# Performance work log

Hardware: AMD Instinct MI355X
Metric: run time of the kernel (lower is better)

## Reference

```python
import jax, jax.numpy as jnp
import numpy as np

B, C_IN, C_OUT, N, K = 4, 128, 128, 4096, 32
BN_EPS = 1e-5


def setup_inputs() -> dict:
    key = jax.random.key(0)
    ks = jax.random.split(key, 12)
    x = jax.random.normal(ks[0], (B, C_IN, N), jnp.float32)
    feature = jax.random.normal(ks[1], (B, C_OUT, N, K), jnp.float32)
    graph_index = jax.random.randint(ks[2], (B, N, K), 0, N)
    s_in = 1.0 / np.sqrt(C_IN)
    s_out = 1.0 / np.sqrt(C_OUT)
    # theta_x: Conv2d(C_IN -> C_IN, 1x1), shared for theta and phi branches
    Wt = jax.random.uniform(ks[3], (C_IN, C_IN), jnp.float32, -s_in, s_in)
    bt = jax.random.uniform(ks[4], (C_IN,), jnp.float32, -s_in, s_in)
    # g: Conv2d(C_OUT -> C_OUT, 1x1)
    Wg = jax.random.uniform(ks[5], (C_OUT, C_OUT), jnp.float32, -s_out, s_out)
    bg = jax.random.uniform(ks[6], (C_OUT,), jnp.float32, -s_out, s_out)
    # W: Conv1d(C_OUT -> C_OUT, 1) followed by BatchNorm1d(C_OUT)
    Ww = jax.random.uniform(ks[7], (C_OUT, C_OUT), jnp.float32, -s_out, s_out)
    bw = jax.random.uniform(ks[8], (C_OUT,), jnp.float32, -s_out, s_out)
    gamma = jnp.ones((C_OUT,), jnp.float32)
    beta = jnp.zeros((C_OUT,), jnp.float32)
    return {"graph_index": graph_index, "x": x, "feature": feature,
            "Wt": Wt, "bt": bt, "Wg": Wg, "bg": bg,
            "Ww": Ww, "bw": bw, "gamma": gamma, "beta": beta}


def reference(graph_index, x, feature, Wt, bt, Wg, bg, Ww, bw, gamma, beta):
    b, c, n = x.shape
    # torch does x.contiguous().view(B, N, C) -> a reshape, not a transpose
    xr = x.reshape(b, n, c)                                   # [B,N,C]
    # index_points: per-batch gather of k neighbors
    batch_idx = jnp.arange(b)[:, None, None]
    nb = xr[batch_idx, graph_index]                           # [B,N,K,C]
    # theta_x 1x1 conv applied to centre and to neighbors (shared weights)
    theta = jnp.einsum('bnc,dc->bnd', xr, Wt) + bt            # [B,N,C]
    phi = jnp.einsum('bnkc,dc->bnkd', nb, Wt) + bt            # [B,N,K,C]
    # local attention logits over k neighbors, softmax over k
    logits = jnp.einsum('bnd,bnkd->bnk', theta, phi)          # [B,N,K]
    coef = jax.nn.softmax(logits, axis=-1)                    # [B,N,K]
    # g 1x1 conv on neighbor value features
    gx = jnp.einsum('bcnk,dc->bnkd', feature, Wg) + bg        # [B,N,K,Cout]
    # weighted aggregation over neighbors
    out = jnp.einsum('bnk,bnkd->bnd', coef, gx)               # [B,N,Cout]
    # W: 1x1 Conv1d then BatchNorm1d (training-mode batch stats)
    y = jnp.einsum('bnd,ed->ben', out, Ww) + bw[None, :, None]  # [B,Cout,N]
    mean = jnp.mean(y, axis=(0, 2), keepdims=True)
    var = jnp.var(y, axis=(0, 2), keepdims=True)
    z = (y - mean) * jax.lax.rsqrt(var + BN_EPS)
    z = z * gamma[None, :, None] + beta[None, :, None]
    return z
```

## Files before the change

kernel.cpp:

```cpp
#include <hip/hip_runtime.h>
#include <hip/hip_bf16.h>

#define BB 4
#define CC 128
#define NN 4096
#define KK 32
#define THETA_OFF 0
#define THETA_SZ  (BB*NN*CC)
#define AGG_OFF   (THETA_OFF + THETA_SZ)
#define AGG_SZ    (BB*NN*CC)
#define M_OFF     (AGG_OFF + AGG_SZ)
#define M_SZ      (CC*CC)
#define B2_OFF    (M_OFF + M_SZ)
#define COEF_OFF  (B2_OFF + 128)
#define COEF_SZ   (BB*NN*KK)
#define PART_OFF  (COEF_OFF + COEF_SZ)
#define PART_SZ   (512*256)
#define PART2_OFF (PART_OFF + PART_SZ)
#define PART2_SZ  (64*256)
#define STAT_OFF  (PART2_OFF + PART2_SZ)

__device__ __forceinline__ float dot4(float4 a, float4 b) {
    return a.x*b.x + a.y*b.y + a.z*b.z + a.w*b.w;
}

__device__ __forceinline__ void async_copy16(const float* g, float* l) {
    __builtin_amdgcn_global_load_lds(
        (const __attribute__((address_space(1))) void*)g,
        (__attribute__((address_space(3))) void*)l, 16, 0, 0);
}

#define SYNCB() do { asm volatile("" ::: "memory"); \
                     __builtin_amdgcn_s_barrier(); \
                     asm volatile("" ::: "memory"); } while (0)

__global__ __launch_bounds__(256) void kWT(const float* __restrict__ x,
                                           const float* __restrict__ Wt,
                                           const float* __restrict__ bt,
                                           const float* __restrict__ Ww,
                                           const float* __restrict__ Wg,
                                           const float* __restrict__ bg,
                                           const float* __restrict__ bw,
                                           float* __restrict__ theta,
                                           float* __restrict__ M,
                                           float* __restrict__ b2) {
    __shared__ float xr[32][132];
    __shared__ float wt[128][36];
    int t = threadIdx.x;
    if (blockIdx.x >= 512) {
        int bid2 = blockIdx.x - 512;
        if (bid2 < 64) {
            int e = bid2 * 2 + (t >> 7);
            int c = t & 127;
            float acc = 0.f;
#pragma unroll 8
            for (int d = 0; d < 128; ++d)
                acc += Ww[e*128 + d] * Wg[d*128 + c];
            M[e*128 + c] = acc;
        } else if (t < 128) {
            float acc = bw[t];
            for (int d = 0; d < 128; ++d)
                acc += Ww[t*128 + d] * bg[d];
            b2[t] = acc;
        }
        return;
    }
    long base = (long)blockIdx.x * (32 * 128);
#pragma unroll
    for (int r = 0; r < 4; ++r) {
        int f = (t + 256*r) * 4;
        int dn = f >> 7, c = f & 127;
        *(float4*)&xr[dn][c] = *(const float4*)(x + base + f);
    }
    float acc[4][4] = {};
    int e0 = t & 31, dn0 = (t >> 5) * 4;
    for (int cb = 0; cb < 4; ++cb) {
        __syncthreads();
#pragma unroll
        for (int r = 0; r < 4; ++r) {
            int f = (t + 256*r) * 4;
            int d = f >> 5, cc = f & 31;
            *(float4*)&wt[d][cc] = *(const float4*)(Wt + d*128 + cb*32 + cc);
        }
        __syncthreads();
#pragma unroll
        for (int q = 0; q < 8; ++q) {
            float4 a4[4], m4[4];
#pragma unroll
            for (int j = 0; j < 4; ++j) a4[j] = *(const float4*)&xr[dn0+j][cb*32 + q*4];
#pragma unroll
            for (int i = 0; i < 4; ++i) m4[i] = *(const float4*)&wt[e0 + 32*i][q*4];
#pragma unroll
            for (int i = 0; i < 4; ++i)
#pragma unroll
                for (int j = 0; j < 4; ++j)
                    acc[i][j] += dot4(a4[j], m4[i]);
        }
    }
    __syncthreads();
#pragma unroll
    for (int i = 0; i < 4; ++i) {
        float b = bt[e0 + 32*i];
#pragma unroll
        for (int j = 0; j < 4; ++j)
            xr[dn0 + j][e0 + 32*i] = acc[i][j] + b;
    }
    __syncthreads();
#pragma unroll
    for (int r = 0; r < 4; ++r) {
        int f = (t + 256*r) * 4;
        int dn = f >> 7, c = f & 127;
        *(float4*)(theta + base + f) = *(const float4*)&xr[dn][c];
    }
}

__global__ __launch_bounds__(256) void kA(const int* __restrict__ gi,
                                          const float* __restrict__ theta,
                                          float* __restrict__ coefG) {
    __shared__ float tc[16][132];
    __shared__ float logits[16][33];
    int t = threadIdx.x;
    int bid = (blockIdx.x & 7) * 128 + (blockIdx.x >> 3);
    long trow0 = (long)bid * 16;
    int b = bid >> 8;
    int k = t >> 3, l8 = t & 7;
#pragma unroll
    for (int r = 0; r < 2; ++r) {
        int f = (t + 256*r) * 4;
        int dn = f >> 7, c = f & 127;
        *(float4*)&tc[dn][c] = *(const float4*)(theta + trow0*128 + f);
    }
    int idxs[16];
#pragma unroll
    for (int dn = 0; dn < 16; ++dn)
        idxs[dn] = gi[(trow0 + dn) * KK + k];
    __syncthreads();
    const float* tbat = theta + (long)b * NN * CC;
#pragma unroll 2
    for (int dn = 0; dn < 16; ++dn) {
        const float* row = tbat + (long)idxs[dn] * CC;
        float p = 0.f;
#pragma unroll
        for (int j = 0; j < 4; ++j) {
            int c = j*32 + l8*4;
            float4 g = *(const float4*)(row + c);
            float4 tcv = *(const float4*)&tc[dn][c];
            p += dot4(g, tcv);
        }
        p += __shfl_xor(p, 1);
        p += __shfl_xor(p, 2);
        p += __shfl_xor(p, 4);
        if (l8 == 0) logits[dn][k] = p;
    }
    __syncthreads();
    if (t < 128) {
        int row = t >> 3;
        float l[4];
#pragma unroll
        for (int j = 0; j < 4; ++j) l[j] = logits[row][l8 + 8*j];
        float m = fmaxf(fmaxf(l[0], l[1]), fmaxf(l[2], l[3]));
        m = fmaxf(m, __shfl_xor(m, 1));
        m = fmaxf(m, __shfl_xor(m, 2));
        m = fmaxf(m, __shfl_xor(m, 4));
        float e[4]; float s = 0.f;
#pragma unroll
        for (int j = 0; j < 4; ++j) { e[j] = __expf(l[j] - m); s += e[j]; }
        s += __shfl_xor(s, 1);
        s += __shfl_xor(s, 2);
        s += __shfl_xor(s, 4);
        float inv = 1.0f / s;
#pragma unroll
        for (int j = 0; j < 4; ++j)
            coefG[(trow0 + row) * KK + l8 + 8*j] = e[j] * inv;
    }
}

__global__ __launch_bounds__(256) void kB(const float* __restrict__ coefG,
                                          const float* __restrict__ feat,
                                          float* __restrict__ aggG) {
    __shared__ float stage[3][4][32][32];
    __shared__ float aggL[32][36];
    int t = threadIdx.x;
    int cc4 = blockIdx.x & 3;
    int tile = blockIdx.x >> 2;
    int b = tile >> 7;
    int n0 = (tile & 127) * 32;
    int dn = t >> 3, l8 = t & 7;
    int w = t >> 6, lane = t & 63;

    float4 cf = *(const float4*)(coefG + ((size_t)tile * 32 + dn) * KK + l8 * 4);
    asm volatile("" :: "v"(cf.x), "v"(cf.y), "v"(cf.z), "v"(cf.w));

    const size_t S = (size_t)NN * KK;
    const float* fbase = feat + ((size_t)b * CC + cc4 * 32) * S + (size_t)n0 * KK + lane * 4;

#pragma unroll
    for (int ch = 0; ch < 3; ++ch) {
        const float* fc = fbase + (size_t)(ch * 4 + w) * S;
        float* ld = &stage[ch][w][0][0];
#pragma unroll
        for (int i = 0; i < 4; ++i)
            async_copy16(fc + i * 256, ld + i * 256);
    }

    int slot = 0;
#pragma unroll
    for (int ch = 0; ch < 8; ++ch) {
        int rem = 7 - ch;
        if (rem >= 2)      asm volatile("s_waitcnt vmcnt(8)" ::: "memory");
        else if (rem == 1) asm volatile("s_waitcnt vmcnt(4)" ::: "memory");
        else               asm volatile("s_waitcnt vmcnt(0)" ::: "memory");
        SYNCB();
#pragma unroll
        for (int cl = 0; cl < 4; ++cl) {
            float4 f = *(const float4*)&stage[slot][cl][dn][l8 * 4];
            float v = dot4(f, cf);
            v += __shfl_xor(v, 1);
            v += __shfl_xor(v, 2);
            v += __shfl_xor(v, 4);
            if (l8 == 0) aggL[dn][ch * 4 + cl] = v;
        }
        SYNCB();
        if (ch + 3 < 8) {
            const float* fc = fbase + (size_t)((ch + 3) * 4 + w) * S;
            float* ld = &stage[slot][w][0][0];
#pragma unroll
            for (int i = 0; i < 4; ++i)
                async_copy16(fc + i * 256, ld + i * 256);
        }
        slot = (slot == 2) ? 0 : slot + 1;
    }
    __syncthreads();
    int row = t >> 3, col4 = l8 * 4;
    *(float4*)(aggG + ((size_t)b * NN + n0 + row) * CC + cc4 * 32 + col4) =
        *(const float4*)&aggL[row][col4];
}

__global__ __launch_bounds__(256) void kC(const float* __restrict__ aggG,
                                          const float* __restrict__ Mmat,
                                          const float* __restrict__ b2v,
                                          float* __restrict__ y,
                                          float* __restrict__ partial) {
    __shared__ float agg[32][132];
    __shared__ float mc[128][36];
    __shared__ float pw[4][128];
    __shared__ float qw[4][128];
    int t = threadIdx.x;
    int b = blockIdx.x >> 7;
    int n0 = (blockIdx.x & 127) * 32;
    long base = (long)blockIdx.x * (32 * 128);
#pragma unroll
    for (int r = 0; r < 4; ++r) {
        int f = (t + 256*r) * 4;
        int dn = f >> 7, c = f & 127;
        *(float4*)&agg[dn][c] = *(const float4*)(aggG + base + f);
    }
    float acc[4][4] = {};
    int e0 = t & 31, dn0 = (t >> 5) * 4;
    for (int cb = 0; cb < 4; ++cb) {
        __syncthreads();
#pragma unroll
        for (int r = 0; r < 4; ++r) {
            int f = (t + 256*r) * 4;
            int e = f >> 5, cc = f & 31;
            *(float4*)&mc[e][cc] = *(const float4*)(Mmat + e*128 + cb*32 + cc);
        }
        __syncthreads();
#pragma unroll
        for (int q = 0; q < 8; ++q) {
            float4 a4[4], m4[4];
#pragma unroll
            for (int j = 0; j < 4; ++j) a4[j] = *(const float4*)&agg[dn0+j][cb*32 + q*4];
#pragma unroll
            for (int i = 0; i < 4; ++i) m4[i] = *(const float4*)&mc[e0 + 32*i][q*4];
#pragma unroll
            for (int i = 0; i < 4; ++i)
#pragma unroll
                for (int j = 0; j < 4; ++j)
                    acc[i][j] += dot4(a4[j], m4[i]);
        }
        __syncthreads();
    }
    int w = t >> 6;
#pragma unroll
    for (int i = 0; i < 4; ++i) {
        int e = e0 + 32*i;
        float bb = b2v[e];
        float4 yv;
        yv.x = acc[i][0] + bb;
        yv.y = acc[i][1] + bb;
        yv.z = acc[i][2] + bb;
        yv.w = acc[i][3] + bb;
        *(float4*)(y + ((long)(b*CC + e)) * NN + n0 + dn0) = yv;
        float s = yv.x + yv.y + yv.z + yv.w;
        float qq = yv.x*yv.x + yv.y*yv.y + yv.z*yv.z + yv.w*yv.w;
        s  += __shfl_xor(s, 32);
        qq += __shfl_xor(qq, 32);
        if (!(t & 32)) { pw[w][e] = s; qw[w][e] = qq; }
    }
    __syncthreads();
    if (t < 128) {
        partial[(long)blockIdx.x * 256 + t]       = pw[0][t] + pw[1][t] + pw[2][t] + pw[3][t];
        partial[(long)blockIdx.x * 256 + 128 + t] = qw[0][t] + qw[1][t] + qw[2][t] + qw[3][t];
    }
}

__global__ __launch_bounds__(256) void kR1(const float* __restrict__ partial,
                                           float* __restrict__ partial2) {
    int t = threadIdx.x;
    long b0 = (long)blockIdx.x * 8;
    float acc = 0.f;
#pragma unroll
    for (int j = 0; j < 8; ++j)
        acc += partial[(b0 + j) * 256 + t];
    partial2[(long)blockIdx.x * 256 + t] = acc;
}

__global__ __launch_bounds__(256) void kR2(const float* __restrict__ partial2,
                                           const float* __restrict__ gamma,
                                           const float* __restrict__ beta,
                                           float* __restrict__ stats) {
    __shared__ float buf[256];
    int t = threadIdx.x;
    float acc = 0.f;
#pragma unroll
    for (int j = 0; j < 64; ++j)
        acc += partial2[j * 256 + t];
    buf[t] = acc;
    __syncthreads();
    if (t < 128) {
        float S = buf[t], Q = buf[t + 128];
        const float invN = 1.0f / (BB * NN);
        float mean = S * invN;
        float var  = Q * invN - mean * mean;
        float sc = rsqrtf(var + 1e-5f) * gamma[t];
        stats[t]       = sc;
        stats[128 + t] = beta[t] - mean * sc;
    }
}

__global__ void kZ(float* __restrict__ y, const float* __restrict__ stats) {
    int idx = blockIdx.x * 256 + threadIdx.x;
#pragma unroll
    for (int r = 0; r < 2; ++r) {
        int i = idx + r * 262144;
        int e = (i >> 10) & 127;
        float sc = stats[e], sh = stats[128 + e];
        float4 v = ((float4*)y)[i];
        v.x = v.x * sc + sh;
        v.y = v.y * sc + sh;
        v.z = v.z * sc + sh;
        v.w = v.w * sc + sh;
        ((float4*)y)[i] = v;
    }
}

extern "C" void kernel_launch(void* const* d_in, const int* in_sizes, int n_in,
                              void* d_out, int out_size, void* d_ws, size_t ws_size,
                              hipStream_t stream) {
    const int*   gi    = (const int*)d_in[0];
    const float* x     = (const float*)d_in[1];
    const float* feat  = (const float*)d_in[2];
    const float* Wt    = (const float*)d_in[3];
    const float* bt    = (const float*)d_in[4];
    const float* Wg    = (const float*)d_in[5];
    const float* bg    = (const float*)d_in[6];
    const float* Ww    = (const float*)d_in[7];
    const float* bw    = (const float*)d_in[8];
    const float* gamma = (const float*)d_in[9];
    const float* beta  = (const float*)d_in[10];

    float* y  = (float*)d_out;
    float* ws = (float*)d_ws;
    float* theta    = ws + THETA_OFF;
    float* aggG     = ws + AGG_OFF;
    float* Mmat     = ws + M_OFF;
    float* b2       = ws + B2_OFF;
    float* coefG    = ws + COEF_OFF;
    float* partial  = ws + PART_OFF;
    float* partial2 = ws + PART2_OFF;
    float* stats    = ws + STAT_OFF;

    kWT<<<577, 256, 0, stream>>>(x, Wt, bt, Ww, Wg, bg, bw, theta, Mmat, b2);
    kA<<<1024, 256, 0, stream>>>(gi, theta, coefG);
    kB<<<2048, 256, 0, stream>>>(coefG, feat, aggG);
    kC<<<512, 256, 0, stream>>>(aggG, Mmat, b2, y, partial);
    kR1<<<64, 256, 0, stream>>>(partial, partial2);
    kR2<<<1, 256, 0, stream>>>(partial2, gamma, beta, stats);
    kZ<<<1024, 256, 0, stream>>>(y, stats);
}
```

Baseline: 107.2 us.

## Fuse neighbor aggregation and output projection into one kernel

Result: slower. 143.5 us (+33.9%).

```diff
diff --git a/kernel.cpp b/kernel.cpp
--- a/kernel.cpp
+++ b/kernel.cpp
@@ -7,9 +7,7 @@
 #define KK 32
 #define THETA_OFF 0
 #define THETA_SZ  (BB*NN*CC)
-#define AGG_OFF   (THETA_OFF + THETA_SZ)
-#define AGG_SZ    (BB*NN*CC)
-#define M_OFF     (AGG_OFF + AGG_SZ)
+#define M_OFF     (THETA_OFF + THETA_SZ)
 #define M_SZ      (CC*CC)
 #define B2_OFF    (M_OFF + M_SZ)
 #define COEF_OFF  (B2_OFF + 128)
@@ -175,14 +173,16 @@
     }
 }
 
-__global__ __launch_bounds__(256) void kB(const float* __restrict__ coefG,
-                                          const float* __restrict__ feat,
-                                          float* __restrict__ aggG) {
+__global__ __launch_bounds__(256) void kBC(const float* __restrict__ coefG,
+                                           const float* __restrict__ feat,
+                                           const float* __restrict__ Mmat,
+                                           const float* __restrict__ b2v,
+                                           float* __restrict__ y,
+                                           float* __restrict__ partial) {
     __shared__ float stage[3][4][32][32];
-    __shared__ float aggL[32][36];
-    int t = threadIdx.x;
-    int cc4 = blockIdx.x & 3;
-    int tile = blockIdx.x >> 2;
+    __shared__ float aggL[32][132];
+    int t = threadIdx.x;
+    int tile = blockIdx.x;
     int b = tile >> 7;
     int n0 = (tile & 127) * 32;
     int dn = t >> 3, l8 = t & 7;
@@ -192,7 +192,7 @@
     asm volatile("" :: "v"(cf.x), "v"(cf.y), "v"(cf.z), "v"(cf.w));
 
     const size_t S = (size_t)NN * KK;
-    const float* fbase = feat + ((size_t)b * CC + cc4 * 32) * S + (size_t)n0 * KK + lane * 4;
+    const float* fbase = feat + (size_t)b * CC * S + (size_t)n0 * KK + lane * 4;
 
 #pragma unroll
     for (int ch = 0; ch < 3; ++ch) {
@@ -205,8 +205,8 @@
 
     int slot = 0;
 #pragma unroll
-    for (int ch = 0; ch < 8; ++ch) {
-        int rem = 7 - ch;
+    for (int ch = 0; ch < 32; ++ch) {
+        int rem = 31 - ch;
         if (rem >= 2)      asm volatile("s_waitcnt vmcnt(8)" ::: "memory");
         else if (rem == 1) asm volatile("s_waitcnt vmcnt(4)" ::: "memory");
         else               asm volatile("s_waitcnt vmcnt(0)" ::: "memory");
@@ -221,7 +221,7 @@
             if (l8 == 0) aggL[dn][ch * 4 + cl] = v;
         }
         SYNCB();
-        if (ch + 3 < 8) {
+        if (ch + 3 < 32) {
             const float* fc = fbase + (size_t)((ch + 3) * 4 + w) * S;
             float* ld = &stage[slot][w][0][0];
 #pragma unroll
@@ -230,31 +230,11 @@
         }
         slot = (slot == 2) ? 0 : slot + 1;
     }
-    __syncthreads();
-    int row = t >> 3, col4 = l8 * 4;
-    *(float4*)(aggG + ((size_t)b * NN + n0 + row) * CC + cc4 * 32 + col4) =
-        *(const float4*)&aggL[row][col4];
-}
-
-__global__ __launch_bounds__(256) void kC(const float* __restrict__ aggG,
-                                          const float* __restrict__ Mmat,
-                                          const float* __restrict__ b2v,
-                                          float* __restrict__ y,
-                                          float* __restrict__ partial) {
-    __shared__ float agg[32][132];
-    __shared__ float mc[128][36];
-    __shared__ float pw[4][128];
-    __shared__ float qw[4][128];
-    int t = threadIdx.x;
-    int b = blockIdx.x >> 7;
-    int n0 = (blockIdx.x & 127) * 32;
-    long base = (long)blockIdx.x * (32 * 128);
-#pragma unroll
-    for (int r = 0; r < 4; ++r) {
-        int f = (t + 256*r) * 4;
-        int dn = f >> 7, c = f & 127;
-        *(float4*)&agg[dn][c] = *(const float4*)(aggG + base + f);
-    }
+
+    float (*mc)[36]  = (float(*)[36])&stage[0][0][0][0];
+    float (*pw)[128] = (float(*)[128])(((float*)stage) + 128*36);
+    float (*qw)[128] = (float(*)[128])(((float*)stage) + 128*36 + 4*128);
+
     float acc[4][4] = {};
     int e0 = t & 31, dn0 = (t >> 5) * 4;
     for (int cb = 0; cb < 4; ++cb) {
@@ -270,7 +250,7 @@
         for (int q = 0; q < 8; ++q) {
             float4 a4[4], m4[4];
 #pragma unroll
-            for (int j = 0; j < 4; ++j) a4[j] = *(const float4*)&agg[dn0+j][cb*32 + q*4];
+            for (int j = 0; j < 4; ++j) a4[j] = *(const float4*)&aggL[dn0+j][cb*32 + q*4];
 #pragma unroll
             for (int i = 0; i < 4; ++i) m4[i] = *(const float4*)&mc[e0 + 32*i][q*4];
 #pragma unroll
@@ -281,7 +261,7 @@
         }
         __syncthreads();
     }
-    int w = t >> 6;
+    int wv = t >> 6;
 #pragma unroll
     for (int i = 0; i < 4; ++i) {
         int e = e0 + 32*i;
@@ -296,12 +276,12 @@
         float qq = yv.x*yv.x + yv.y*yv.y + yv.z*yv.z + yv.w*yv.w;
         s  += __shfl_xor(s, 32);
         qq += __shfl_xor(qq, 32);
-        if (!(t & 32)) { pw[w][e] = s; qw[w][e] = qq; }
+        if (!(t & 32)) { pw[wv][e] = s; qw[wv][e] = qq; }
     }
     __syncthreads();
     if (t < 128) {
-        partial[(long)blockIdx.x * 256 + t]       = pw[0][t] + pw[1][t] + pw[2][t] + pw[3][t];
-        partial[(long)blockIdx.x * 256 + 128 + t] = qw[0][t] + qw[1][t] + qw[2][t] + qw[3][t];
+        partial[(long)tile * 256 + t]       = pw[0][t] + pw[1][t] + pw[2][t] + pw[3][t];
+        partial[(long)tile * 256 + 128 + t] = qw[0][t] + qw[1][t] + qw[2][t] + qw[3][t];
     }
 }
 
@@ -373,7 +353,6 @@
     float* y  = (float*)d_out;
     float* ws = (float*)d_ws;
     float* theta    = ws + THETA_OFF;
-    float* aggG     = ws + AGG_OFF;
     float* Mmat     = ws + M_OFF;
     float* b2       = ws + B2_OFF;
     float* coefG    = ws + COEF_OFF;
@@ -383,8 +362,7 @@
 
     kWT<<<577, 256, 0, stream>>>(x, Wt, bt, Ww, Wg, bg, bw, theta, Mmat, b2);
     kA<<<1024, 256, 0, stream>>>(gi, theta, coefG);
-    kB<<<2048, 256, 0, stream>>>(coefG, feat, aggG);
-    kC<<<512, 256, 0, stream>>>(aggG, Mmat, b2, y, partial);
+    kBC<<<512, 256, 0, stream>>>(coefG, feat, Mmat, b2, y, partial);
     kR1<<<64, 256, 0, stream>>>(partial, partial2);
     kR2<<<1, 256, 0, stream>>>(partial2, gamma, beta, stats);
     kZ<<<1024, 256, 0, stream>>>(y, stats);
```

## Fuse BN stats finalize into normalize kernel and shrink kB pipeline to double-buffer

Applied to the files above, without the earlier changes.

Result: faster. 102.5 us (-4.4%).

```diff
diff --git a/kernel.cpp b/kernel.cpp
--- a/kernel.cpp
+++ b/kernel.cpp
@@ -18,7 +18,6 @@
 #define PART_SZ   (512*256)
 #define PART2_OFF (PART_OFF + PART_SZ)
 #define PART2_SZ  (64*256)
-#define STAT_OFF  (PART2_OFF + PART2_SZ)
 
 __device__ __forceinline__ float dot4(float4 a, float4 b) {
     return a.x*b.x + a.y*b.y + a.z*b.z + a.w*b.w;
@@ -178,7 +177,7 @@
 __global__ __launch_bounds__(256) void kB(const float* __restrict__ coefG,
                                           const float* __restrict__ feat,
                                           float* __restrict__ aggG) {
-    __shared__ float stage[3][4][32][32];
+    __shared__ float stage[2][4][32][32];
     __shared__ float aggL[32][36];
     int t = threadIdx.x;
     int cc4 = blockIdx.x & 3;
@@ -195,7 +194,7 @@
     const float* fbase = feat + ((size_t)b * CC + cc4 * 32) * S + (size_t)n0 * KK + lane * 4;
 
 #pragma unroll
-    for (int ch = 0; ch < 3; ++ch) {
+    for (int ch = 0; ch < 2; ++ch) {
         const float* fc = fbase + (size_t)(ch * 4 + w) * S;
         float* ld = &stage[ch][w][0][0];
 #pragma unroll
@@ -206,10 +205,8 @@
     int slot = 0;
 #pragma unroll
     for (int ch = 0; ch < 8; ++ch) {
-        int rem = 7 - ch;
-        if (rem >= 2)      asm volatile("s_waitcnt vmcnt(8)" ::: "memory");
-        else if (rem == 1) asm volatile("s_waitcnt vmcnt(4)" ::: "memory");
-        else               asm volatile("s_waitcnt vmcnt(0)" ::: "memory");
+        if (ch < 7) asm volatile("s_waitcnt vmcnt(4)" ::: "memory");
+        else        asm volatile("s_waitcnt vmcnt(0)" ::: "memory");
         SYNCB();
 #pragma unroll
         for (int cl = 0; cl < 4; ++cl) {
@@ -221,14 +218,14 @@
             if (l8 == 0) aggL[dn][ch * 4 + cl] = v;
         }
         SYNCB();
-        if (ch + 3 < 8) {
-            const float* fc = fbase + (size_t)((ch + 3) * 4 + w) * S;
+        if (ch + 2 < 8) {
+            const float* fc = fbase + (size_t)((ch + 2) * 4 + w) * S;
             float* ld = &stage[slot][w][0][0];
 #pragma unroll
             for (int i = 0; i < 4; ++i)
                 async_copy16(fc + i * 256, ld + i * 256);
         }
-        slot = (slot == 2) ? 0 : slot + 1;
+        slot ^= 1;
     }
     __syncthreads();
     int row = t >> 3, col4 = l8 * 4;
@@ -316,14 +313,16 @@
     partial2[(long)blockIdx.x * 256 + t] = acc;
 }
 
-__global__ __launch_bounds__(256) void kR2(const float* __restrict__ partial2,
+__global__ __launch_bounds__(256) void kZf(float* __restrict__ y,
+                                           const float* __restrict__ partial2,
                                            const float* __restrict__ gamma,
-                                           const float* __restrict__ beta,
-                                           float* __restrict__ stats) {
+                                           const float* __restrict__ beta) {
     __shared__ float buf[256];
+    __shared__ float scs[128];
+    __shared__ float shs[128];
     int t = threadIdx.x;
     float acc = 0.f;
-#pragma unroll
+#pragma unroll 8
     for (int j = 0; j < 64; ++j)
         acc += partial2[j * 256 + t];
     buf[t] = acc;
@@ -334,18 +333,16 @@
         float mean = S * invN;
         float var  = Q * invN - mean * mean;
         float sc = rsqrtf(var + 1e-5f) * gamma[t];
-        stats[t]       = sc;
-        stats[128 + t] = beta[t] - mean * sc;
-    }
-}
-
-__global__ void kZ(float* __restrict__ y, const float* __restrict__ stats) {
-    int idx = blockIdx.x * 256 + threadIdx.x;
+        scs[t] = sc;
+        shs[t] = beta[t] - mean * sc;
+    }
+    __syncthreads();
+    int idx = blockIdx.x * 256 + t;
 #pragma unroll
     for (int r = 0; r < 2; ++r) {
         int i = idx + r * 262144;
         int e = (i >> 10) & 127;
-        float sc = stats[e], sh = stats[128 + e];
+        float sc = scs[e], sh = shs[e];
         float4 v = ((float4*)y)[i];
         v.x = v.x * sc + sh;
         v.y = v.y * sc + sh;
@@ -379,13 +376,11 @@
     float* coefG    = ws + COEF_OFF;
     float* partial  = ws + PART_OFF;
     float* partial2 = ws + PART2_OFF;
-    float* stats    = ws + STAT_OFF;
 
     kWT<<<577, 256, 0, stream>>>(x, Wt, bt, Ww, Wg, bg, bw, theta, Mmat, b2);
     kA<<<1024, 256, 0, stream>>>(gi, theta, coefG);
     kB<<<2048, 256, 0, stream>>>(coefG, feat, aggG);
     kC<<<512, 256, 0, stream>>>(aggG, Mmat, b2, y, partial);
     kR1<<<64, 256, 0, stream>>>(partial, partial2);
-    kR2<<<1, 256, 0, stream>>>(partial2, gamma, beta, stats);
-    kZ<<<1024, 256, 0, stream>>>(y, stats);
-}
+    kZf<<<1024, 256, 0, stream>>>(y, partial2, gamma, beta);
+}
```
